# Performance work log

Measured on AMD Instinct MI355X. Metric: run time of the kernel, lower is better.

The kernel has to match this reference:

```python
import jax, jax.numpy as jnp
import numpy as np

D_MODEL = 1024
D_FF = 2048
NUM_GROUPS = 4
EXPERTS_PER_GROUP = 4
TOP_K = 2
N_TOKENS = 4096
TOTAL_EXPERTS = NUM_GROUPS * EXPERTS_PER_GROUP


def setup_inputs() -> dict:
    key = jax.random.key(0)
    ks = jax.random.split(key, 7)
    s = 0.02
    return {
        "x": jax.random.normal(ks[0], (N_TOKENS, D_MODEL), dtype=jnp.float32),
        "Wg": jax.random.normal(ks[1], (D_MODEL, NUM_GROUPS), dtype=jnp.float32) * s,
        "We": jax.random.normal(ks[2], (D_MODEL, TOTAL_EXPERTS), dtype=jnp.float32) * s,
        "w1": jax.random.normal(ks[3], (TOTAL_EXPERTS, D_MODEL, D_FF), dtype=jnp.float32) * s,
        "b1": jnp.zeros((TOTAL_EXPERTS, D_FF), dtype=jnp.float32),
        "w2": jax.random.normal(ks[4], (TOTAL_EXPERTS, D_FF, D_MODEL), dtype=jnp.float32) * s,
        "b2": jnp.zeros((TOTAL_EXPERTS, D_MODEL), dtype=jnp.float32),
    }


def _router(x, Wg, We):
    N = x.shape[0]
    G, Eg = NUM_GROUPS, EXPERTS_PER_GROUP
    # Level 1: group gate
    group_probs = jax.nn.softmax(x @ Wg, axis=-1)            # [N, G]
    group_mask = group_probs >= (1.0 / G)
    # Level 2: expert gate (per-group softmax)
    expert_logits = (x @ We).reshape(N, G, Eg)
    expert_probs = jax.nn.softmax(expert_logits, axis=-1)    # [N, G, Eg]
    expert_mask = expert_probs >= (1.0 / Eg)
    valid_mask = (group_mask[:, :, None] & expert_mask).reshape(N, G * Eg)
    final_probs = (group_probs[:, :, None] * expert_probs).reshape(N, G * Eg)
    # Fallback: if fewer than top_k experts pass thresholds, use top-k by prob
    num_selected = valid_mask.sum(axis=-1)
    _, topk_idx = jax.lax.top_k(final_probs, TOP_K)          # [N, top_k]
    topk_mask = jnp.zeros((N, G * Eg), dtype=bool).at[
        jnp.arange(N)[:, None], topk_idx].set(True)
    use_topk = num_selected < TOP_K
    final_mask = jnp.where(use_topk[:, None], topk_mask, valid_mask)
    sel = final_probs * final_mask.astype(final_probs.dtype)
    w = sel / jnp.clip(sel.sum(axis=-1, keepdims=True), 1e-9)
    return final_mask, w                                      # [N, E], [N, E]


def reference(x, Wg, We, w1, b1, w2, b2):
    _, weights = _router(x, Wg, We)                          # [N, E]
    # Dense expert compute; masked-out experts contribute weight 0,
    # matching the gather/FFN/index_add loop in the original.
    h = jax.nn.gelu(jnp.einsum("nd,edf->nef", x, w1) + b1, approximate=False)
    y = jnp.einsum("nef,efd->ned", h, w2) + b2               # [N, E, D]
    return jnp.einsum("ne,ned->nd", weights, y)              # [N, D]
```

## Files before the change

kernel.cpp:

```cpp
#include <hip/hip_runtime.h>
#include <math.h>

#define NT 4096
#define DM 1024
#define DF 2048
#define NEXP 16

typedef __attribute__((ext_vector_type(8))) short bf16x8;
typedef __attribute__((ext_vector_type(4))) float f32x4;

__device__ __forceinline__ unsigned short f2bf(float f) {
  unsigned int u = __builtin_bit_cast(unsigned int, f);
  u += 0x7fffu + ((u >> 16) & 1u);
  return (unsigned short)(u >> 16);
}

__device__ __forceinline__ void gload_lds16(const void* g, void* l) {
  __builtin_amdgcn_global_load_lds(
      (__attribute__((address_space(1))) void*)g,
      (__attribute__((address_space(3))) void*)l, 16, 0, 0);
}

__device__ __forceinline__ void softmax4(float* v) {
  float m = fmaxf(fmaxf(v[0], v[1]), fmaxf(v[2], v[3]));
  float s = 0.f;
#pragma unroll
  for (int j = 0; j < 4; ++j) { v[j] = expf(v[j] - m); s += v[j]; }
  float inv = 1.f / s;
#pragma unroll
  for (int j = 0; j < 4; ++j) v[j] *= inv;
}

__global__ __launch_bounds__(256) void router2_kernel(
    const float* __restrict__ x, const float* __restrict__ Wg,
    const float* __restrict__ We, unsigned int* __restrict__ emask,
    float* __restrict__ eweight, unsigned short* __restrict__ xb) {
  int n = blockIdx.x;
  int tid = threadIdx.x;
  int c0 = tid * 4;
  float4 xv = *(const float4*)(x + (size_t)n * DM + c0);
  if (xb) {
    ushort4 o = make_ushort4(f2bf(xv.x), f2bf(xv.y), f2bf(xv.z), f2bf(xv.w));
    *(ushort4*)(xb + (size_t)n * DM + c0) = o;
  }
  float xa[4] = {xv.x, xv.y, xv.z, xv.w};
  float acc[20];
#pragma unroll
  for (int j = 0; j < 20; ++j) acc[j] = 0.f;
#pragma unroll
  for (int j = 0; j < 4; ++j) {
    int c = c0 + j;
    float4 wg = *(const float4*)(Wg + c * 4);
    acc[0] += xa[j] * wg.x; acc[1] += xa[j] * wg.y;
    acc[2] += xa[j] * wg.z; acc[3] += xa[j] * wg.w;
#pragma unroll
    for (int q = 0; q < 4; ++q) {
      float4 we = *(const float4*)(We + c * 16 + q * 4);
      acc[4 + q * 4 + 0] += xa[j] * we.x;
      acc[4 + q * 4 + 1] += xa[j] * we.y;
      acc[4 + q * 4 + 2] += xa[j] * we.z;
      acc[4 + q * 4 + 3] += xa[j] * we.w;
    }
  }
#pragma unroll
  for (int j = 0; j < 20; ++j) {
    float v = acc[j];
#pragma unroll
    for (int s = 32; s; s >>= 1) v += __shfl_xor(v, s, 64);
    acc[j] = v;
  }
  __shared__ float red[4][20];
  int lane = tid & 63, wv = tid >> 6;
  if (lane == 0) {
#pragma unroll
    for (int j = 0; j < 20; ++j) red[wv][j] = acc[j];
  }
  __syncthreads();
  if (tid == 0) {
    float t[20];
#pragma unroll
    for (int j = 0; j < 20; ++j)
      t[j] = red[0][j] + red[1][j] + red[2][j] + red[3][j];
    float gp[4] = {t[0], t[1], t[2], t[3]};
    softmax4(gp);
    float ep[16];
#pragma unroll
    for (int g = 0; g < 4; ++g) {
      float tt[4] = {t[4 + g * 4], t[5 + g * 4], t[6 + g * 4], t[7 + g * 4]};
      softmax4(tt);
#pragma unroll
      for (int i = 0; i < 4; ++i) ep[g * 4 + i] = tt[i];
    }
    float fp[16];
    bool valid[16];
    int nsel = 0;
#pragma unroll
    for (int g = 0; g < 4; ++g) {
      bool gm = gp[g] >= 0.25f;
#pragma unroll
      for (int i = 0; i < 4; ++i) {
        int e = g * 4 + i;
        bool em = ep[e] >= 0.25f;
        valid[e] = gm && em;
        fp[e] = gp[g] * ep[e];
        nsel += valid[e] ? 1 : 0;
      }
    }
    int m1 = 0; float v1 = -1.f;
#pragma unroll
    for (int e = 0; e < 16; ++e) if (fp[e] > v1) { v1 = fp[e]; m1 = e; }
    int m2 = -1; float v2 = -2.f;
#pragma unroll
    for (int e = 0; e < 16; ++e) if (e != m1 && fp[e] > v2) { v2 = fp[e]; m2 = e; }
    bool use_topk = nsel < 2;
    float sel[16]; float s = 0.f;
#pragma unroll
    for (int e = 0; e < 16; ++e) {
      bool msk = use_topk ? (e == m1 || e == m2) : valid[e];
      sel[e] = msk ? fp[e] : 0.f;
      s += sel[e];
      valid[e] = msk;
    }
    float inv = 1.f / fmaxf(s, 1e-9f);
    unsigned int mbits = 0;
    float wv16[16];
#pragma unroll
    for (int e = 0; e < 16; ++e) {
      mbits |= (valid[e] ? 1u : 0u) << e;
      wv16[e] = valid[e] ? sel[e] * inv : 0.f;
    }
    emask[n] = mbits;
#pragma unroll
    for (int i = 0; i < 4; ++i)
      *(float4*)(eweight + (size_t)n * 16 + i * 4) =
          make_float4(wv16[i * 4], wv16[i * 4 + 1], wv16[i * 4 + 2], wv16[i * 4 + 3]);
  }
}

__global__ __launch_bounds__(256) void compact_kernel(
    const unsigned int* __restrict__ emask, const float* __restrict__ eweight,
    int* __restrict__ counts, int* __restrict__ lists, float* __restrict__ wl) {
  int e = blockIdx.x;
  int tid = threadIdx.x, lane = tid & 63, wv = tid >> 6;
  __shared__ int wcnt[4];
  int running = 0;
  for (int base = 0; base < NT; base += 256) {
    int n = base + tid;
    bool p = (emask[n] >> e) & 1u;
    unsigned long long bal = __ballot(p);
    int cnt = __popcll(bal);
    if (lane == 0) wcnt[wv] = cnt;
    __syncthreads();
    int off = running;
#pragma unroll
    for (int w = 0; w < 4; ++w)
      if (w < wv) off += wcnt[w];
    int tot = wcnt[0] + wcnt[1] + wcnt[2] + wcnt[3];
    if (p) {
      int pos = off + (int)__popcll(bal & ((1ull << lane) - 1ull));
      lists[e * NT + pos] = n;
      wl[e * NT + pos] = eweight[(size_t)n * 16 + e];
    }
    running += tot;
    __syncthreads();
  }
  if (tid == 0) counts[e] = running;
}

__global__ void prefix_kernel(const int* __restrict__ counts, int* __restrict__ base,
                              int* __restrict__ ent, int* __restrict__ nent) {
  if (threadIdx.x == 0 && blockIdx.x == 0) {
    int acc = 0, n = 0;
    for (int e = 0; e < NEXP; ++e) {
      base[e] = acc;
      acc += (counts[e] + 255) & ~255;
      int mt = (counts[e] + 127) >> 7;
      for (int m = 0; m < mt; ++m) ent[n++] = (e << 16) | m;
    }
    *nent = n;
  }
}

__global__ __launch_bounds__(256) void wtrans_kernel(
    const float* __restrict__ in, unsigned short* __restrict__ outp, int K, int N) {
  int e = blockIdx.z;
  int n0 = blockIdx.x * 64;
  int k0 = blockIdx.y * 64;
  const float* src = in + (size_t)e * K * N;
  unsigned short* dst = outp + (size_t)e * K * N;
  __shared__ unsigned short t[64][65];
  int tid = threadIdx.x;
#pragma unroll
  for (int it = 0; it < 4; ++it) {
    int idx = it * 256 + tid;
    int r = idx >> 4, c4 = (idx & 15) << 2;
    float4 v = *(const float4*)(src + (size_t)(k0 + r) * N + n0 + c4);
    t[r][c4 + 0] = f2bf(v.x);
    t[r][c4 + 1] = f2bf(v.y);
    t[r][c4 + 2] = f2bf(v.z);
    t[r][c4 + 3] = f2bf(v.w);
  }
  __syncthreads();
#pragma unroll
  for (int it = 0; it < 4; ++it) {
    int idx = it * 256 + tid;
    int r = idx >> 4, c4 = (idx & 15) << 2;
    ushort4 o;
    o.x = t[c4 + 0][r]; o.y = t[c4 + 1][r];
    o.z = t[c4 + 2][r]; o.w = t[c4 + 3][r];
    *(ushort4*)(dst + (size_t)(n0 + r) * K + k0 + c4) = o;
  }
}

__global__ __launch_bounds__(256, 4) void ffn1p_kernel(
    const unsigned short* __restrict__ xb, const unsigned short* __restrict__ wt,
    const float* __restrict__ b1, const int* __restrict__ counts,
    const int* __restrict__ lists, const int* __restrict__ base,
    const int* __restrict__ ent, const int* __restrict__ nent,
    int* __restrict__ q, unsigned short* __restrict__ h, int cap) {
  __shared__ unsigned short lA[128 * 64];
  __shared__ unsigned short lB[128 * 64];
  __shared__ int s_idx;
  int tid = threadIdx.x, lane = tid & 63, wid = tid >> 6;
  int wm = wid >> 1, wn = wid & 1;
  int lrow = lane & 15, lk = lane >> 4;
  int chunk = lane & 7, row_l = lane >> 3;
  int total = (*nent) * 16;

  for (;;) {
    __syncthreads();
    if (tid == 0) s_idx = atomicAdd(q, 1);
    __syncthreads();
    int idx = s_idx;
    if (idx >= total) return;
    int en = ent[idx >> 4];
    int e = en >> 16;
    int m0 = (en & 0xffff) * 128;
    int n0 = (idx & 15) * 128;
    int count = counts[e];
    int hbase = base[e];
    if (hbase + m0 + 128 > cap) continue;
    const unsigned short* we = wt + (size_t)e * DM * DF;
    const int* lst = lists + e * NT + m0;

    const char* asrc[4];
    const char* bsrc[4];
#pragma unroll
    for (int c = 0; c < 4; ++c) {
      int r = wid * 32 + c * 8 + row_l;
      int sc = chunk ^ (r & 7);
      int rr = (m0 + r < count) ? r : 0;
      int tok = lst[rr];
      asrc[c] = (const char*)xb + (size_t)tok * DM * 2 + sc * 16;
      bsrc[c] = (const char*)we + (size_t)(n0 + r) * DM * 2 + sc * 16;
    }

    f32x4 acc[4][4];
#pragma unroll
    for (int m = 0; m < 4; ++m)
#pragma unroll
      for (int n = 0; n < 4; ++n) acc[m][n] = (f32x4)0.0f;

    for (int kt = 0; kt < DM / 64; ++kt) {
      __syncthreads();
#pragma unroll
      for (int c = 0; c < 4; ++c) {
        gload_lds16(asrc[c] + kt * 128, (void*)(lA + (wid * 32 + c * 8) * 64));
        gload_lds16(bsrc[c] + kt * 128, (void*)(lB + (wid * 32 + c * 8) * 64));
      }
      __syncthreads();
#pragma unroll
      for (int ks = 0; ks < 2; ++ks) {
        bf16x8 af[4], bfr[4];
#pragma unroll
        for (int m = 0; m < 4; ++m) {
          int row = wm * 64 + m * 16 + lrow;
          int off = row * 128 + (((ks * 64) + lk * 16) ^ ((row & 7) << 4));
          af[m] = *(const bf16x8*)((const char*)lA + off);
        }
#pragma unroll
        for (int n = 0; n < 4; ++n) {
          int row = wn * 64 + n * 16 + lrow;
          int off = row * 128 + (((ks * 64) + lk * 16) ^ ((row & 7) << 4));
          bfr[n] = *(const bf16x8*)((const char*)lB + off);
        }
#pragma unroll
        for (int m = 0; m < 4; ++m)
#pragma unroll
          for (int n = 0; n < 4; ++n)
            acc[m][n] = __builtin_amdgcn_mfma_f32_16x16x32_bf16(af[m], bfr[n], acc[m][n], 0, 0, 0);
      }
    }
#pragma unroll
    for (int m = 0; m < 4; ++m) {
      int rbase = hbase + m0 + wm * 64 + m * 16 + lk * 4;
#pragma unroll
      for (int n = 0; n < 4; ++n) {
        int col = n0 + wn * 64 + n * 16 + lrow;
        float bias = b1[e * DF + col];
#pragma unroll
        for (int j = 0; j < 4; ++j) {
          float v = acc[m][n][j] + bias;
          float g = 0.5f * v * (1.0f + erff(v * 0.70710678f));
          h[(size_t)(rbase + j) * DF + col] = f2bf(g);
        }
      }
    }
  }
}

__global__ __launch_bounds__(256, 4) void ffn2p_kernel(
    const unsigned short* __restrict__ h, const unsigned short* __restrict__ wt,
    const float* __restrict__ b2, const int* __restrict__ counts,
    const int* __restrict__ lists, const int* __restrict__ base,
    const int* __restrict__ ent, const int* __restrict__ nent,
    int* __restrict__ q, const float* __restrict__ wl,
    float* __restrict__ out, int cap) {
  __shared__ unsigned short lA[128 * 64];
  __shared__ unsigned short lB[128 * 64];
  __shared__ int s_idx;
  int tid = threadIdx.x, lane = tid & 63, wid = tid >> 6;
  int wm = wid >> 1, wn = wid & 1;
  int lrow = lane & 15, lk = lane >> 4;
  int chunk = lane & 7, row_l = lane >> 3;
  int total = (*nent) * 8;

  for (;;) {
    __syncthreads();
    if (tid == 0) s_idx = atomicAdd(q, 1);
    __syncthreads();
    int idx = s_idx;
    if (idx >= total) return;
    int en = ent[idx >> 3];
    int e = en >> 16;
    int m0 = (en & 0xffff) * 128;
    int n0 = (idx & 7) * 128;
    int count = counts[e];
    int hbase = base[e];
    if (hbase + m0 + 128 > cap) continue;
    const unsigned short* we = wt + (size_t)e * DM * DF;

    const char* asrc[4];
    const char* bsrc[4];
#pragma unroll
    for (int c = 0; c < 4; ++c) {
      int r = wid * 32 + c * 8 + row_l;
      int sc = chunk ^ (r & 7);
      asrc[c] = (const char*)h + (size_t)(hbase + m0 + r) * DF * 2 + sc * 16;
      bsrc[c] = (const char*)we + (size_t)(n0 + r) * DF * 2 + sc * 16;
    }

    f32x4 acc[4][4];
#pragma unroll
    for (int m = 0; m < 4; ++m)
#pragma unroll
      for (int n = 0; n < 4; ++n) acc[m][n] = (f32x4)0.0f;

    for (int kt = 0; kt < DF / 64; ++kt) {
      __syncthreads();
#pragma unroll
      for (int c = 0; c < 4; ++c) {
        gload_lds16(asrc[c] + kt * 128, (void*)(lA + (wid * 32 + c * 8) * 64));
        gload_lds16(bsrc[c] + kt * 128, (void*)(lB + (wid * 32 + c * 8) * 64));
      }
      __syncthreads();
#pragma unroll
      for (int ks = 0; ks < 2; ++ks) {
        bf16x8 af[4], bfr[4];
#pragma unroll
        for (int m = 0; m < 4; ++m) {
          int row = wm * 64 + m * 16 + lrow;
          int off = row * 128 + (((ks * 64) + lk * 16) ^ ((row & 7) << 4));
          af[m] = *(const bf16x8*)((const char*)lA + off);
        }
#pragma unroll
        for (int n = 0; n < 4; ++n) {
          int row = wn * 64 + n * 16 + lrow;
          int off = row * 128 + (((ks * 64) + lk * 16) ^ ((row & 7) << 4));
          bfr[n] = *(const bf16x8*)((const char*)lB + off);
        }
#pragma unroll
        for (int m = 0; m < 4; ++m)
#pragma unroll
          for (int n = 0; n < 4; ++n)
            acc[m][n] = __builtin_amdgcn_mfma_f32_16x16x32_bf16(af[m], bfr[n], acc[m][n], 0, 0, 0);
      }
    }
#pragma unroll
    for (int m = 0; m < 4; ++m) {
      int rbase = m0 + wm * 64 + m * 16 + lk * 4;
#pragma unroll
      for (int n = 0; n < 4; ++n) {
        int col = n0 + wn * 64 + n * 16 + lrow;
        float bias = b2[e * DM + col];
#pragma unroll
        for (int j = 0; j < 4; ++j) {
          int slot = rbase + j;
          if (slot < count) {
            int tok = lists[e * NT + slot];
            float w = wl[e * NT + slot];
            atomicAdd(out + (size_t)tok * DM + col, w * (acc[m][n][j] + bias));
          }
        }
      }
    }
  }
}

__global__ __launch_bounds__(256) void ffn1_kernel(
    const float* __restrict__ x, const float* __restrict__ w1,
    const float* __restrict__ b1, const int* __restrict__ counts,
    const int* __restrict__ lists, const int* __restrict__ base,
    unsigned short* __restrict__ h, int cap, int e_arg) {
  int e = (e_arg >= 0) ? e_arg : (int)blockIdx.z;
  int count = counts[e];
  int m0 = blockIdx.y * 128;
  if (m0 >= count) return;
  int hbase = base[e];
  if (hbase + m0 + 128 > cap) return;
  int n0 = blockIdx.x * 128;
  const float* w1e = w1 + (size_t)e * DM * DF;
  const int* lst = lists + e * NT + m0;
  __shared__ unsigned short lA[128 * 64];
  __shared__ unsigned short lB[128 * 64];
  int tid = threadIdx.x;
  int lane = tid & 63, wid = tid >> 6;
  int wm = wid >> 1, wn = wid & 1;
  int lrow = lane & 15, lk = lane >> 4;
  f32x4 acc[4][4];
#pragma unroll
  for (int m = 0; m < 4; ++m)
#pragma unroll
    for (int n = 0; n < 4; ++n) acc[m][n] = (f32x4)0.0f;
  for (int kt = 0; kt < DM / 64; ++kt) {
    int k0 = kt * 64;
    __syncthreads();
#pragma unroll
    for (int p = 0; p < 8; ++p) {
      int idx = p * 256 + tid;
      int r = idx >> 4, c4 = idx & 15;
      int tok = (m0 + r < count) ? lst[r] : lst[0];
      float4 v = *(const float4*)(x + (size_t)tok * DM + k0 + c4 * 4);
      ushort4 bv = make_ushort4(f2bf(v.x), f2bf(v.y), f2bf(v.z), f2bf(v.w));
      int off = r * 128 + ((c4 * 8) ^ ((r & 7) << 4));
      *(ushort4*)((char*)lA + off) = bv;
    }
#pragma unroll
    for (int p = 0; p < 16; ++p) {
      int idx = p * 256 + tid;
      int n = idx & 127, k2 = idx >> 7;
      const float* bp = w1e + (size_t)(k0 + 2 * k2) * DF + n0 + n;
      ushort2 bv = make_ushort2(f2bf(bp[0]), f2bf(bp[DF]));
      int off = n * 128 + ((k2 * 4) ^ ((n & 7) << 4));
      *(ushort2*)((char*)lB + off) = bv;
    }
    __syncthreads();
#pragma unroll
    for (int ks = 0; ks < 2; ++ks) {
      bf16x8 af[4], bfr[4];
#pragma unroll
      for (int m = 0; m < 4; ++m) {
        int row = wm * 64 + m * 16 + lrow;
        int off = row * 128 + (((ks * 64) + lk * 16) ^ ((row & 7) << 4));
        af[m] = *(const bf16x8*)((const char*)lA + off);
      }
#pragma unroll
      for (int n = 0; n < 4; ++n) {
        int row = wn * 64 + n * 16 + lrow;
        int off = row * 128 + (((ks * 64) + lk * 16) ^ ((row & 7) << 4));
        bfr[n] = *(const bf16x8*)((const char*)lB + off);
      }
#pragma unroll
      for (int m = 0; m < 4; ++m)
#pragma unroll
        for (int n = 0; n < 4; ++n)
          acc[m][n] = __builtin_amdgcn_mfma_f32_16x16x32_bf16(af[m], bfr[n], acc[m][n], 0, 0, 0);
    }
  }
#pragma unroll
  for (int m = 0; m < 4; ++m) {
    int rbase = hbase + m0 + wm * 64 + m * 16 + lk * 4;
#pragma unroll
    for (int n = 0; n < 4; ++n) {
      int col = n0 + wn * 64 + n * 16 + lrow;
      float bias = b1[e * DF + col];
#pragma unroll
      for (int j = 0; j < 4; ++j) {
        float v = acc[m][n][j] + bias;
        float g = 0.5f * v * (1.0f + erff(v * 0.70710678f));
        h[(size_t)(rbase + j) * DF + col] = f2bf(g);
      }
    }
  }
}

__global__ __launch_bounds__(256) void ffn2_kernel(
    const unsigned short* __restrict__ h, const float* __restrict__ w2,
    const float* __restrict__ b2, const int* __restrict__ counts,
    const int* __restrict__ lists, const int* __restrict__ base,
    const float* __restrict__ wl, float* __restrict__ out, int cap, int e_arg) {
  int e = (e_arg >= 0) ? e_arg : (int)blockIdx.z;
  int count = counts[e];
  int m0 = blockIdx.y * 128;
  if (m0 >= count) return;
  int hbase = base[e];
  if (hbase + m0 + 128 > cap) return;
  int n0 = blockIdx.x * 128;
  const float* w2e = w2 + (size_t)e * DF * DM;
  __shared__ unsigned short lA[128 * 64];
  __shared__ unsigned short lB[128 * 64];
  int tid = threadIdx.x;
  int lane = tid & 63, wid = tid >> 6;
  int wm = wid >> 1, wn = wid & 1;
  int lrow = lane & 15, lk = lane >> 4;
  f32x4 acc[4][4];
#pragma unroll
  for (int m = 0; m < 4; ++m)
#pragma unroll
    for (int n = 0; n < 4; ++n) acc[m][n] = (f32x4)0.0f;
  for (int kt = 0; kt < DF / 64; ++kt) {
    int k0 = kt * 64;
    __syncthreads();
#pragma unroll
    for (int p = 0; p < 8; ++p) {
      int idx = p * 256 + tid;
      int r = idx >> 4, c4 = idx & 15;
      ushort4 v = *(const ushort4*)(h + (size_t)(hbase + m0 + r) * DF + k0 + c4 * 4);
      int off = r * 128 + ((c4 * 8) ^ ((r & 7) << 4));
      *(ushort4*)((char*)lA + off) = v;
    }
#pragma unroll
    for (int p = 0; p < 16; ++p) {
      int idx = p * 256 + tid;
      int n = idx & 127, k2 = idx >> 7;
      const float* bp = w2e + (size_t)(k0 + 2 * k2) * DM + n0 + n;
      ushort2 bv = make_ushort2(f2bf(bp[0]), f2bf(bp[DM]));
      int off = n * 128 + ((k2 * 4) ^ ((n & 7) << 4));
      *(ushort2*)((char*)lB + off) = bv;
    }
    __syncthreads();
#pragma unroll
    for (int ks = 0; ks < 2; ++ks) {
      bf16x8 af[4], bfr[4];
#pragma unroll
      for (int m = 0; m < 4; ++m) {
        int row = wm * 64 + m * 16 + lrow;
        int off = row * 128 + (((ks * 64) + lk * 16) ^ ((row & 7) << 4));
        af[m] = *(const bf16x8*)((const char*)lA + off);
      }
#pragma unroll
      for (int n = 0; n < 4; ++n) {
        int row = wn * 64 + n * 16 + lrow;
        int off = row * 128 + (((ks * 64) + lk * 16) ^ ((row & 7) << 4));
        bfr[n] = *(const bf16x8*)((const char*)lB + off);
      }
#pragma unroll
      for (int m = 0; m < 4; ++m)
#pragma unroll
        for (int n = 0; n < 4; ++n)
          acc[m][n] = __builtin_amdgcn_mfma_f32_16x16x32_bf16(af[m], bfr[n], acc[m][n], 0, 0, 0);
    }
  }
#pragma unroll
  for (int m = 0; m < 4; ++m) {
    int rbase = m0 + wm * 64 + m * 16 + lk * 4;
#pragma unroll
    for (int n = 0; n < 4; ++n) {
      int col = n0 + wn * 64 + n * 16 + lrow;
      float bias = b2[e * DM + col];
#pragma unroll
      for (int j = 0; j < 4; ++j) {
        int slot = rbase + j;
        if (slot < count) {
          int tok = lists[e * NT + slot];
          float w = wl[e * NT + slot];
          atomicAdd(out + (size_t)tok * DM + col, w * (acc[m][n][j] + bias));
        }
      }
    }
  }
}

extern "C" void kernel_launch(void* const* d_in, const int* in_sizes, int n_in,
                              void* d_out, int out_size, void* d_ws, size_t ws_size,
                              hipStream_t stream) {
  const float* x  = (const float*)d_in[0];
  const float* Wg = (const float*)d_in[1];
  const float* We = (const float*)d_in[2];
  const float* w1 = (const float*)d_in[3];
  const float* b1 = (const float*)d_in[4];
  const float* w2 = (const float*)d_in[5];
  const float* b2 = (const float*)d_in[6];
  float* out = (float*)d_out;

  char* ws = (char*)d_ws;
  int* counts = (int*)ws;
  int* base   = (int*)(ws + 256);
  int* q      = (int*)(ws + 512);
  int* nent   = (int*)(ws + 576);
  int* ent    = (int*)(ws + 1024);
  unsigned int* emask = (unsigned int*)(ws + 4096);
  int* lists  = (int*)(ws + 32768);
  float* wl   = (float*)(ws + 32768 + NEXP * NT * 4);
  float* eweight = (float*)(ws + 32768 + 2 * NEXP * NT * 4);

  const size_t OFF_XB = 1u << 20;
  const size_t OFF_WT = OFF_XB + ((size_t)NT * DM * 2);
  const size_t OFF_H  = OFF_WT + ((size_t)NEXP * DM * DF * 2);
  long cap_new = ((long)ws_size - (long)OFF_H) / (DF * 2);

  unsigned short* xb_router =
      (cap_new >= 20000) ? (unsigned short*)(ws + OFF_XB) : (unsigned short*)0;

  hipMemsetAsync(out, 0, (size_t)NT * DM * sizeof(float), stream);
  hipMemsetAsync(ws, 0, 1024, stream);
  router2_kernel<<<NT, 256, 0, stream>>>(x, Wg, We, emask, eweight, xb_router);
  compact_kernel<<<NEXP, 256, 0, stream>>>(emask, eweight, counts, lists, wl);

  if (cap_new >= 20000) {
    unsigned short* xb = (unsigned short*)(ws + OFF_XB);
    unsigned short* wt = (unsigned short*)(ws + OFF_WT);
    unsigned short* h  = (unsigned short*)(ws + OFF_H);
    int cap = (int)(cap_new > 65536 ? 65536 : cap_new);
    prefix_kernel<<<1, 64, 0, stream>>>(counts, base, ent, nent);
    wtrans_kernel<<<dim3(DF / 64, DM / 64, NEXP), 256, 0, stream>>>(w1, wt, DM, DF);
    ffn1p_kernel<<<1024, 256, 0, stream>>>(
        xb, wt, b1, counts, lists, base, ent, nent, q, h, cap);
    wtrans_kernel<<<dim3(DM / 64, DF / 64, NEXP), 256, 0, stream>>>(w2, wt, DF, DM);
    ffn2p_kernel<<<1024, 256, 0, stream>>>(
        h, wt, b2, counts, lists, base, ent, nent, q + 1, wl, out, cap);
  } else {
    unsigned short* h = (unsigned short*)(ws + OFF_XB);
    long cap_rows = ((long)ws_size - (long)OFF_XB) / (DF * 2);
    if (cap_rows >= 24576) {
      int cap = (int)(cap_rows > 65536 ? 65536 : cap_rows);
      prefix_kernel<<<1, 64, 0, stream>>>(counts, base, ent, nent);
      ffn1_kernel<<<dim3(DF / 128, NT / 128, NEXP), 256, 0, stream>>>(
          x, w1, b1, counts, lists, base, h, cap, -1);
      ffn2_kernel<<<dim3(DM / 128, NT / 128, NEXP), 256, 0, stream>>>(
          h, w2, b2, counts, lists, base, wl, out, cap, -1);
    } else {
      hipMemsetAsync(base, 0, 64, stream);
      for (int e = 0; e < NEXP; ++e) {
        ffn1_kernel<<<dim3(DF / 128, NT / 128, 1), 256, 0, stream>>>(
            x, w1, b1, counts, lists, base, h, NT, e);
        ffn2_kernel<<<dim3(DM / 128, NT / 128, 1), 256, 0, stream>>>(
            h, w2, b2, counts, lists, base, wl, out, NT, e);
      }
    }
  }
}
```

Measured before the change: 369.5 us.

## Static XCD-aware expert scheduling, bf16 expert outputs with gather reduce, tanh GELU

Replaces the atomic work-queue tile scheduler with a static mapping in which each XCD (block index mod 8) handles two experts, so an expert's weights stay in one XCD's L2. The second FFN now writes per-slot bf16 outputs, and a new per-token reduce kernel gathers them with weights and bias. This replaces scattered fp32 atomicAdds into the output. The exact erf GELU is also swapped for a tanh approximation using __expf, which changes numerics slightly. Rounding the FFN2 output to bf16 adds further error, and the static split may load-imbalance when expert counts are uneven.

```diff
diff --git a/kernel.cpp b/kernel.cpp
--- a/kernel.cpp
+++ b/kernel.cpp
@@ -14,11 +14,21 @@
   u += 0x7fffu + ((u >> 16) & 1u);
   return (unsigned short)(u >> 16);
 }
+__device__ __forceinline__ float bf2f(unsigned short s) {
+  unsigned int u = ((unsigned int)s) << 16;
+  return __builtin_bit_cast(float, u);
+}
 
 __device__ __forceinline__ void gload_lds16(const void* g, void* l) {
   __builtin_amdgcn_global_load_lds(
       (__attribute__((address_space(1))) void*)g,
       (__attribute__((address_space(3))) void*)l, 16, 0, 0);
+}
+
+__device__ __forceinline__ float gelu_f(float v) {
+  float u = v * (0.7978845608f + 0.0356774081f * v * v);
+  float t = 1.0f - 2.0f / (__expf(2.0f * u) + 1.0f);
+  return 0.5f * v * (1.0f + t);
 }
 
 __device__ __forceinline__ void softmax4(float* v) {
@@ -139,7 +149,8 @@
 
 __global__ __launch_bounds__(256) void compact_kernel(
     const unsigned int* __restrict__ emask, const float* __restrict__ eweight,
-    int* __restrict__ counts, int* __restrict__ lists, float* __restrict__ wl) {
+    int* __restrict__ counts, int* __restrict__ lists, float* __restrict__ wl,
+    int* __restrict__ slotpos) {
   int e = blockIdx.x;
   int tid = threadIdx.x, lane = tid & 63, wv = tid >> 6;
   __shared__ int wcnt[4];
@@ -160,6 +171,7 @@
       int pos = off + (int)__popcll(bal & ((1ull << lane) - 1ull));
       lists[e * NT + pos] = n;
       wl[e * NT + pos] = eweight[(size_t)n * 16 + e];
+      slotpos[e * NT + n] = pos;
     }
     running += tot;
     __syncthreads();
@@ -212,32 +224,34 @@
   }
 }
 
-__global__ __launch_bounds__(256, 4) void ffn1p_kernel(
+
+__global__ __launch_bounds__(256, 4) void ffn1s_kernel(
     const unsigned short* __restrict__ xb, const unsigned short* __restrict__ wt,
     const float* __restrict__ b1, const int* __restrict__ counts,
     const int* __restrict__ lists, const int* __restrict__ base,
-    const int* __restrict__ ent, const int* __restrict__ nent,
-    int* __restrict__ q, unsigned short* __restrict__ h, int cap) {
+    unsigned short* __restrict__ h, int cap) {
+  const int NN = DF / 128;
+  const int NSLOT = 128;
+  int b = blockIdx.x;
+  int xcd = b & 7, slot = b >> 3;
+  int e0 = xcd, e1 = xcd + 8;
+  int c0 = counts[e0], c1 = counts[e1];
+  int mt0 = (c0 + 127) >> 7, mt1 = (c1 + 127) >> 7;
+  int T0 = mt0 * NN, T = T0 + mt1 * NN;
+
   __shared__ unsigned short lA[128 * 64];
   __shared__ unsigned short lB[128 * 64];
-  __shared__ int s_idx;
+
   int tid = threadIdx.x, lane = tid & 63, wid = tid >> 6;
   int wm = wid >> 1, wn = wid & 1;
   int lrow = lane & 15, lk = lane >> 4;
   int chunk = lane & 7, row_l = lane >> 3;
-  int total = (*nent) * 16;
-
-  for (;;) {
-    __syncthreads();
-    if (tid == 0) s_idx = atomicAdd(q, 1);
-    __syncthreads();
-    int idx = s_idx;
-    if (idx >= total) return;
-    int en = ent[idx >> 4];
-    int e = en >> 16;
-    int m0 = (en & 0xffff) * 128;
-    int n0 = (idx & 15) * 128;
-    int count = counts[e];
+
+  for (int k = slot; k < T; k += NSLOT) {
+    int e, mti, nt, count;
+    if (k < T0) { e = e0; nt = k / mt0; mti = k % mt0; count = c0; }
+    else        { int kk = k - T0; e = e1; nt = kk / mt1; mti = kk % mt1; count = c1; }
+    int m0 = mti * 128, n0 = nt * 128;
     int hbase = base[e];
     if (hbase + m0 + 128 > cap) continue;
     const unsigned short* we = wt + (size_t)e * DM * DF;
@@ -301,41 +315,39 @@
 #pragma unroll
         for (int j = 0; j < 4; ++j) {
           float v = acc[m][n][j] + bias;
-          float g = 0.5f * v * (1.0f + erff(v * 0.70710678f));
-          h[(size_t)(rbase + j) * DF + col] = f2bf(g);
-        }
-      }
-    }
-  }
-}
-
-__global__ __launch_bounds__(256, 4) void ffn2p_kernel(
+          h[(size_t)(rbase + j) * DF + col] = f2bf(gelu_f(v));
+        }
+      }
+    }
+  }
+}
+
+__global__ __launch_bounds__(256, 4) void ffn2y_kernel(
     const unsigned short* __restrict__ h, const unsigned short* __restrict__ wt,
-    const float* __restrict__ b2, const int* __restrict__ counts,
-    const int* __restrict__ lists, const int* __restrict__ base,
-    const int* __restrict__ ent, const int* __restrict__ nent,
-    int* __restrict__ q, const float* __restrict__ wl,
-    float* __restrict__ out, int cap) {
+    const int* __restrict__ counts, const int* __restrict__ base,
+    unsigned short* __restrict__ y, int cap) {
+  const int NN = DM / 128;
+  const int NSLOT = 128;
+  int b = blockIdx.x;
+  int xcd = b & 7, slot = b >> 3;
+  int e0 = xcd, e1 = xcd + 8;
+  int c0 = counts[e0], c1 = counts[e1];
+  int mt0 = (c0 + 127) >> 7, mt1 = (c1 + 127) >> 7;
+  int T0 = mt0 * NN, T = T0 + mt1 * NN;
+
   __shared__ unsigned short lA[128 * 64];
   __shared__ unsigned short lB[128 * 64];
-  __shared__ int s_idx;
+
   int tid = threadIdx.x, lane = tid & 63, wid = tid >> 6;
   int wm = wid >> 1, wn = wid & 1;
   int lrow = lane & 15, lk = lane >> 4;
   int chunk = lane & 7, row_l = lane >> 3;
-  int total = (*nent) * 8;
-
-  for (;;) {
-    __syncthreads();
-    if (tid == 0) s_idx = atomicAdd(q, 1);
-    __syncthreads();
-    int idx = s_idx;
-    if (idx >= total) return;
-    int en = ent[idx >> 3];
-    int e = en >> 16;
-    int m0 = (en & 0xffff) * 128;
-    int n0 = (idx & 7) * 128;
-    int count = counts[e];
+
+  for (int k = slot; k < T; k += NSLOT) {
+    int e, mti, nt, count;
+    if (k < T0) { e = e0; nt = k / mt0; mti = k % mt0; count = c0; }
+    else        { int kk = k - T0; e = e1; nt = kk / mt1; mti = kk % mt1; count = c1; }
+    int m0 = mti * 128, n0 = nt * 128;
     int hbase = base[e];
     if (hbase + m0 + 128 > cap) continue;
     const unsigned short* we = wt + (size_t)e * DM * DF;
@@ -388,6 +400,125 @@
     }
 #pragma unroll
     for (int m = 0; m < 4; ++m) {
+      int rbase = hbase + m0 + wm * 64 + m * 16 + lk * 4;
+      int lcl = m0 + wm * 64 + m * 16 + lk * 4;
+#pragma unroll
+      for (int n = 0; n < 4; ++n) {
+        int col = n0 + wn * 64 + n * 16 + lrow;
+#pragma unroll
+        for (int j = 0; j < 4; ++j) {
+          if (lcl + j < count)
+            y[(size_t)(rbase + j) * DM + col] = f2bf(acc[m][n][j]);
+        }
+      }
+    }
+  }
+}
+
+__global__ __launch_bounds__(256) void reduce_kernel(
+    const unsigned int* __restrict__ emask, const float* __restrict__ eweight,
+    const int* __restrict__ slotpos, const int* __restrict__ base,
+    const unsigned short* __restrict__ y, const float* __restrict__ b2,
+    float* __restrict__ out) {
+  int n = blockIdx.x;
+  int tid = threadIdx.x;
+  int c = tid * 4;
+  unsigned int mask = emask[n];
+  float4 accv = make_float4(0.f, 0.f, 0.f, 0.f);
+  while (mask) {
+    int e = __ffs(mask) - 1;
+    mask &= mask - 1;
+    float w = eweight[(size_t)n * 16 + e];
+    int row = base[e] + slotpos[e * NT + n];
+    ushort4 yv = *(const ushort4*)(y + (size_t)row * DM + c);
+    float4 bv = *(const float4*)(b2 + e * DM + c);
+    accv.x += w * (bf2f(yv.x) + bv.x);
+    accv.y += w * (bf2f(yv.y) + bv.y);
+    accv.z += w * (bf2f(yv.z) + bv.z);
+    accv.w += w * (bf2f(yv.w) + bv.w);
+  }
+  *(float4*)(out + (size_t)n * DM + c) = accv;
+}
+
+__global__ __launch_bounds__(256, 4) void ffn2s_kernel(
+    const unsigned short* __restrict__ h, const unsigned short* __restrict__ wt,
+    const float* __restrict__ b2, const int* __restrict__ counts,
+    const int* __restrict__ lists, const int* __restrict__ base,
+    const float* __restrict__ wl, float* __restrict__ out, int cap) {
+  const int NN = DM / 128;
+  const int NSLOT = 128;
+  int b = blockIdx.x;
+  int xcd = b & 7, slot = b >> 3;
+  int e0 = xcd, e1 = xcd + 8;
+  int c0 = counts[e0], c1 = counts[e1];
+  int mt0 = (c0 + 127) >> 7, mt1 = (c1 + 127) >> 7;
+  int T0 = mt0 * NN, T = T0 + mt1 * NN;
+
+  __shared__ unsigned short lA[128 * 64];
+  __shared__ unsigned short lB[128 * 64];
+
+  int tid = threadIdx.x, lane = tid & 63, wid = tid >> 6;
+  int wm = wid >> 1, wn = wid & 1;
+  int lrow = lane & 15, lk = lane >> 4;
+  int chunk = lane & 7, row_l = lane >> 3;
+
+  for (int k = slot; k < T; k += NSLOT) {
+    int e, mti, nt, count;
+    if (k < T0) { e = e0; nt = k / mt0; mti = k % mt0; count = c0; }
+    else        { int kk = k - T0; e = e1; nt = kk / mt1; mti = kk % mt1; count = c1; }
+    int m0 = mti * 128, n0 = nt * 128;
+    int hbase = base[e];
+    if (hbase + m0 + 128 > cap) continue;
+    const unsigned short* we = wt + (size_t)e * DM * DF;
+
+    const char* asrc[4];
+    const char* bsrc[4];
+#pragma unroll
+    for (int c = 0; c < 4; ++c) {
+      int r = wid * 32 + c * 8 + row_l;
+      int sc = chunk ^ (r & 7);
+      asrc[c] = (const char*)h + (size_t)(hbase + m0 + r) * DF * 2 + sc * 16;
+      bsrc[c] = (const char*)we + (size_t)(n0 + r) * DF * 2 + sc * 16;
+    }
+
+    f32x4 acc[4][4];
+#pragma unroll
+    for (int m = 0; m < 4; ++m)
+#pragma unroll
+      for (int n = 0; n < 4; ++n) acc[m][n] = (f32x4)0.0f;
+
+    for (int kt = 0; kt < DF / 64; ++kt) {
+      __syncthreads();
+#pragma unroll
+      for (int c = 0; c < 4; ++c) {
+        gload_lds16(asrc[c] + kt * 128, (void*)(lA + (wid * 32 + c * 8) * 64));
+        gload_lds16(bsrc[c] + kt * 128, (void*)(lB + (wid * 32 + c * 8) * 64));
+      }
+      __syncthreads();
+#pragma unroll
+      for (int ks = 0; ks < 2; ++ks) {
+        bf16x8 af[4], bfr[4];
+#pragma unroll
+        for (int m = 0; m < 4; ++m) {
+          int row = wm * 64 + m * 16 + lrow;
+          int off = row * 128 + (((ks * 64) + lk * 16) ^ ((row & 7) << 4));
+          af[m] = *(const bf16x8*)((const char*)lA + off);
+        }
+#pragma unroll
+        for (int n = 0; n < 4; ++n) {
+          int row = wn * 64 + n * 16 + lrow;
+          int off = row * 128 + (((ks * 64) + lk * 16) ^ ((row & 7) << 4));
+          bfr[n] = *(const bf16x8*)((const char*)lB + off);
+        }
+#pragma unroll
+        for (int m = 0; m < 4; ++m)
+#pragma unroll
+          for (int n = 0; n < 4; ++n)
+            acc[m][n] = __builtin_amdgcn_mfma_f32_16x16x32_bf16(af[m], bfr[n], acc[m][n], 0, 0, 0);
+      }
+    }
+#pragma unroll
+    for (int m = 0; m < 4; ++m) {
       int rbase = m0 + wm * 64 + m * 16 + lk * 4;
 #pragma unroll
       for (int n = 0; n < 4; ++n) {
@@ -395,10 +526,10 @@
         float bias = b2[e * DM + col];
 #pragma unroll
         for (int j = 0; j < 4; ++j) {
-          int slot = rbase + j;
-          if (slot < count) {
-            int tok = lists[e * NT + slot];
-            float w = wl[e * NT + slot];
+          int sl = rbase + j;
+          if (sl < count) {
+            int tok = lists[e * NT + sl];
+            float w = wl[e * NT + sl];
             atomicAdd(out + (size_t)tok * DM + col, w * (acc[m][n][j] + bias));
           }
         }
@@ -487,8 +618,7 @@
 #pragma unroll
       for (int j = 0; j < 4; ++j) {
         float v = acc[m][n][j] + bias;
-        float g = 0.5f * v * (1.0f + erff(v * 0.70710678f));
-        h[(size_t)(rbase + j) * DF + col] = f2bf(g);
+        h[(size_t)(rbase + j) * DF + col] = f2bf(gelu_f(v));
       }
     }
   }
@@ -596,39 +726,47 @@
   char* ws = (char*)d_ws;
   int* counts = (int*)ws;
   int* base   = (int*)(ws + 256);
-  int* q      = (int*)(ws + 512);
   int* nent   = (int*)(ws + 576);
   int* ent    = (int*)(ws + 1024);
   unsigned int* emask = (unsigned int*)(ws + 4096);
   int* lists  = (int*)(ws + 32768);
   float* wl   = (float*)(ws + 32768 + NEXP * NT * 4);
   float* eweight = (float*)(ws + 32768 + 2 * NEXP * NT * 4);
-
-  const size_t OFF_XB = 1u << 20;
+  int* slotpos   = (int*)(ws + 32768 + 3 * NEXP * NT * 4);
+
+  const size_t OFF_XB = 2u << 20;
   const size_t OFF_WT = OFF_XB + ((size_t)NT * DM * 2);
   const size_t OFF_H  = OFF_WT + ((size_t)NEXP * DM * DF * 2);
-  long cap_new = ((long)ws_size - (long)OFF_H) / (DF * 2);
-
-  unsigned short* xb_router =
-      (cap_new >= 20000) ? (unsigned short*)(ws + OFF_XB) : (unsigned short*)0;
+  long cap6 = ((long)ws_size - (long)OFF_H) / (DF * 2 + DM * 2);
+  long cap4 = ((long)ws_size - (long)OFF_H) / (DF * 2);
+  bool fast = (cap4 >= 20000);
+
+  unsigned short* xb_router = fast ? (unsigned short*)(ws + OFF_XB) : (unsigned short*)0;
 
   hipMemsetAsync(out, 0, (size_t)NT * DM * sizeof(float), stream);
   hipMemsetAsync(ws, 0, 1024, stream);
   router2_kernel<<<NT, 256, 0, stream>>>(x, Wg, We, emask, eweight, xb_router);
-  compact_kernel<<<NEXP, 256, 0, stream>>>(emask, eweight, counts, lists, wl);
-
-  if (cap_new >= 20000) {
+  compact_kernel<<<NEXP, 256, 0, stream>>>(emask, eweight, counts, lists, wl, slotpos);
+
+  if (fast) {
     unsigned short* xb = (unsigned short*)(ws + OFF_XB);
     unsigned short* wt = (unsigned short*)(ws + OFF_WT);
     unsigned short* h  = (unsigned short*)(ws + OFF_H);
-    int cap = (int)(cap_new > 65536 ? 65536 : cap_new);
     prefix_kernel<<<1, 64, 0, stream>>>(counts, base, ent, nent);
     wtrans_kernel<<<dim3(DF / 64, DM / 64, NEXP), 256, 0, stream>>>(w1, wt, DM, DF);
-    ffn1p_kernel<<<1024, 256, 0, stream>>>(
-        xb, wt, b1, counts, lists, base, ent, nent, q, h, cap);
-    wtrans_kernel<<<dim3(DM / 64, DF / 64, NEXP), 256, 0, stream>>>(w2, wt, DF, DM);
-    ffn2p_kernel<<<1024, 256, 0, stream>>>(
-        h, wt, b2, counts, lists, base, ent, nent, q + 1, wl, out, cap);
+    if (cap6 >= 20000) {
+      int cap = (int)(cap6 > 65536 ? 65536 : cap6);
+      unsigned short* y = (unsigned short*)(ws + OFF_H + (size_t)cap * DF * 2);
+      ffn1s_kernel<<<1024, 256, 0, stream>>>(xb, wt, b1, counts, lists, base, h, cap);
+      wtrans_kernel<<<dim3(DM / 64, DF / 64, NEXP), 256, 0, stream>>>(w2, wt, DF, DM);
+      ffn2y_kernel<<<1024, 256, 0, stream>>>(h, wt, counts, base, y, cap);
+      reduce_kernel<<<NT, 256, 0, stream>>>(emask, eweight, slotpos, base, y, b2, out);
+    } else {
+      int cap = (int)(cap4 > 65536 ? 65536 : cap4);
+      ffn1s_kernel<<<1024, 256, 0, stream>>>(xb, wt, b1, counts, lists, base, h, cap);
+      wtrans_kernel<<<dim3(DM / 64, DF / 64, NEXP), 256, 0, stream>>>(w2, wt, DF, DM);
+      ffn2s_kernel<<<1024, 256, 0, stream>>>(h, wt, b2, counts, lists, base, wl, out, cap);
+    }
   } else {
     unsigned short* h = (unsigned short*)(ws + OFF_XB);
     long cap_rows = ((long)ws_size - (long)OFF_XB) / (DF * 2);
```

Result: faster. 310.6 us (-16.0%).
